# Kernel tuning notes

Hardware: AMD Instinct MI355X
Metric: run time of the kernel (lower is better)

Reference implementation:

```python
import jax, jax.numpy as jnp
import numpy as np

T, B, IN, H, OUT = 4096, 64, 4, 256, 2


def setup_inputs() -> dict:
    key = jax.random.key(0)
    ks = jax.random.split(key, 8)
    k = (1.0 / H) ** 0.5
    return {
        "input": jax.random.normal(ks[0], (T, B, IN), dtype=jnp.float32),
        "target": jax.random.normal(ks[1], (T, B, OUT), dtype=jnp.float32),
        "Wi": jax.random.uniform(ks[2], (H, IN), minval=-k, maxval=k, dtype=jnp.float32),
        "bi": jax.random.uniform(ks[3], (H,), minval=-k, maxval=k, dtype=jnp.float32),
        "Wh": jax.random.uniform(ks[4], (H, H), minval=-k, maxval=k, dtype=jnp.float32),
        "bh": jax.random.uniform(ks[5], (H,), minval=-k, maxval=k, dtype=jnp.float32),
        "Wf": jax.random.normal(ks[6], (OUT, H), dtype=jnp.float32) * (1.0 / H) ** 0.5,
        "bf": jnp.zeros((OUT,), dtype=jnp.float32),
    }


def reference(input, target, Wi, bi, Wh, bh, Wf, bf):
    # Precompute input projection for all timesteps: [T, B, H]
    xi = jnp.einsum("tbi,hi->tbh", input, Wi) + bi

    def step(h, xt):
        # h: [B, H]; xt: [B, H] (already projected input)
        h_new = jnp.tanh(xt + h @ Wh.T + bh)
        return h_new, h_new

    h0 = jnp.zeros((input.shape[1], Wh.shape[0]), dtype=input.dtype)
    _, hs = jax.lax.scan(step, h0, xi)  # hs: [T, B, H]

    # Output head: tanh(Linear(hidden)) -> [T, B, OUT]
    out = jnp.tanh(jnp.einsum("tbh,oh->tbo", hs, Wf) + bf)
    return out
```

## Files before the change

kernel.cpp:

```cpp
#include <hip/hip_runtime.h>

#define T_STEPS 4096
#define BATCH   64
#define INDIM   4
#define H       256
#define OUTD    2
#define CHUNK   32
#define SLOT_DW 36
#define ENT_DW  (4*SLOT_DW)
#define ENT_B   (4*ENT_DW)
#define RING_DW (CHUNK*ENT_DW)
#define WF_DW   (OUTD*(H/2))
#define XS_DW   (CHUNK*INDIM)

typedef __fp16 half2v __attribute__((ext_vector_type(2)));

__device__ __forceinline__ float fast_tanh(float x) {
    float ax = fabsf(x);
    float e  = __expf(-2.0f * ax);
    float r  = (1.0f - e) * __builtin_amdgcn_rcpf(1.0f + e);
    return copysignf(r, x);
}

template<int CTRL>
__device__ __forceinline__ float qadd(float a) {
    int s = __builtin_amdgcn_update_dpp(0, __builtin_bit_cast(int, a),
                                        CTRL, 0xf, 0xf, true);
    return a + __builtin_bit_cast(float, s);
}
#define QX1 0xB1
#define QX2 0x4E

__global__ __attribute__((amdgpu_waves_per_eu(1, 1))) __launch_bounds__(256)
void elman_kernel(const float* __restrict__ input,
                  const float* __restrict__ Wi,
                  const float* __restrict__ bi,
                  const float* __restrict__ Wh,
                  const float* __restrict__ bh,
                  const float* __restrict__ Wf,
                  const float* __restrict__ bf,
                  float* __restrict__ out)
{
    const int b  = blockIdx.x;
    const int t  = threadIdx.x;
    const int q  = t >> 2;
    const int ko = t & 3;
    const int k0 = ko * 64;

    __shared__ unsigned int lds[RING_DW + WF_DW + XS_DW];
    unsigned int* ring   = lds;
    unsigned int* wf_pk  = lds + RING_DW;
    float*        xstage = (float*)(lds + RING_DW + WF_DW);

    half2v w[4][32];
    #pragma unroll
    for (int r = 0; r < 4; ++r) {
        const float* p = Wh + (size_t)(4 * q + r) * H + k0;
        #pragma unroll
        for (int j = 0; j < 16; ++j) {
            float4 a = *(const float4*)(p + 4 * j);
            w[r][2 * j]     = __builtin_amdgcn_cvt_pkrtz(a.x, a.y);
            w[r][2 * j + 1] = __builtin_amdgcn_cvt_pkrtz(a.z, a.w);
        }
    }
    #pragma unroll
    for (int r = 0; r < 4; ++r)
        #pragma unroll
        for (int j = 0; j < 32; ++j) {
            float f = __builtin_bit_cast(float, w[r][j]);
            asm volatile("" : "+v"(f));
            w[r][j] = __builtin_bit_cast(half2v, f);
        }

    const float4 wim   = *(const float4*)(Wi + t * INDIM);
    const float  biasm = bi[t] + bh[t];
    const float  bf0   = bf[0], bf1 = bf[1];
    const int    boff  = (t >> 6) * (SLOT_DW * 4) + (t & 63) * 2;

    {
        const int o = t >> 7, e = t & 127;
        wf_pk[t] = __builtin_bit_cast(unsigned int,
            __builtin_amdgcn_cvt_pkrtz(Wf[o * H + 2 * e], Wf[o * H + 2 * e + 1]));
    }
    if (t < H / 2) ring[(CHUNK - 1) * ENT_DW + (t >> 5) * SLOT_DW + (t & 31)] = 0u;
    __syncthreads();

    const unsigned int rd_off = (unsigned int)(ko * SLOT_DW);

    for (int chunk = 0; chunk < T_STEPS / CHUNK; ++chunk) {
        if (t < CHUNK) {
            const int s = chunk * CHUNK + t;
            ((float4*)xstage)[t] = *(const float4*)(input + ((size_t)s * BATCH + b) * INDIM);
        }
        __syncthreads();

        #pragma unroll 1
        for (int i = 0; i < CHUNK; ++i) {
            const unsigned int* hb =
                ring + ((i + CHUNK - 1) & (CHUNK - 1)) * ENT_DW + rd_off;
            uint4 hv[8];
            #pragma unroll
            for (int j = 0; j < 8; ++j) hv[j] = *(const uint4*)(hb + 4 * j);
            const float4 xs = *((const float4*)xstage + i);

            float acc0 = 0.f, acc1 = 0.f, acc2 = 0.f, acc3 = 0.f;
            #pragma unroll
            for (int j = 0; j < 8; ++j) {
                half2v h0 = __builtin_bit_cast(half2v, hv[j].x);
                half2v h1 = __builtin_bit_cast(half2v, hv[j].y);
                half2v h2 = __builtin_bit_cast(half2v, hv[j].z);
                half2v h3 = __builtin_bit_cast(half2v, hv[j].w);
                acc0 = __builtin_amdgcn_fdot2(w[0][4 * j],     h0, acc0, false);
                acc1 = __builtin_amdgcn_fdot2(w[1][4 * j],     h0, acc1, false);
                acc2 = __builtin_amdgcn_fdot2(w[2][4 * j],     h0, acc2, false);
                acc3 = __builtin_amdgcn_fdot2(w[3][4 * j],     h0, acc3, false);
                acc0 = __builtin_amdgcn_fdot2(w[0][4 * j + 1], h1, acc0, false);
                acc1 = __builtin_amdgcn_fdot2(w[1][4 * j + 1], h1, acc1, false);
                acc2 = __builtin_amdgcn_fdot2(w[2][4 * j + 1], h1, acc2, false);
                acc3 = __builtin_amdgcn_fdot2(w[3][4 * j + 1], h1, acc3, false);
                acc0 = __builtin_amdgcn_fdot2(w[0][4 * j + 2], h2, acc0, false);
                acc1 = __builtin_amdgcn_fdot2(w[1][4 * j + 2], h2, acc1, false);
                acc2 = __builtin_amdgcn_fdot2(w[2][4 * j + 2], h2, acc2, false);
                acc3 = __builtin_amdgcn_fdot2(w[3][4 * j + 2], h2, acc3, false);
                acc0 = __builtin_amdgcn_fdot2(w[0][4 * j + 3], h3, acc0, false);
                acc1 = __builtin_amdgcn_fdot2(w[1][4 * j + 3], h3, acc1, false);
                acc2 = __builtin_amdgcn_fdot2(w[2][4 * j + 3], h3, acc2, false);
                acc3 = __builtin_amdgcn_fdot2(w[3][4 * j + 3], h3, acc3, false);
            }

            acc0 = qadd<QX1>(acc0);
            acc1 = qadd<QX1>(acc1);
            acc2 = qadd<QX1>(acc2);
            acc3 = qadd<QX1>(acc3);
            float A  = (ko & 1) ? acc1 : acc0;
            float Bv = (ko & 1) ? acc3 : acc2;
            A  = qadd<QX2>(A);
            Bv = qadd<QX2>(Bv);
            float accm = (ko & 2) ? Bv : A;

            float pre = accm + biasm +
                xs.x * wim.x + xs.y * wim.y + xs.z * wim.z + xs.w * wim.w;
            __fp16 h16 = (__fp16)fast_tanh(pre);
            *(__fp16*)((char*)ring + i * ENT_B + boff) = h16;

            __syncthreads();
        }

        {
            const int task = t >> 2;
            const int s    = task >> 1;
            const int o    = task & 1;
            const int sub  = t & 3;
            const unsigned int* hp = ring + s * ENT_DW + sub * SLOT_DW;
            const unsigned int* wp = wf_pk + o * (H / 2) + sub * 32;

            float acc = 0.f;
            #pragma unroll
            for (int j = 0; j < 8; ++j) {
                uint4 hq = *(const uint4*)(hp + 4 * j);
                uint4 wq = *(const uint4*)(wp + 4 * j);
                acc = __builtin_amdgcn_fdot2(__builtin_bit_cast(half2v, wq.x),
                                             __builtin_bit_cast(half2v, hq.x), acc, false);
                acc = __builtin_amdgcn_fdot2(__builtin_bit_cast(half2v, wq.y),
                                             __builtin_bit_cast(half2v, hq.y), acc, false);
                acc = __builtin_amdgcn_fdot2(__builtin_bit_cast(half2v, wq.z),
                                             __builtin_bit_cast(half2v, hq.z), acc, false);
                acc = __builtin_amdgcn_fdot2(__builtin_bit_cast(half2v, wq.w),
                                             __builtin_bit_cast(half2v, hq.w), acc, false);
            }
            acc = qadd<QX1>(acc);
            acc = qadd<QX2>(acc);

            if (sub == 0) {
                out[((size_t)(chunk * CHUNK + s) * BATCH + b) * OUTD + o] =
                    fast_tanh(acc + (o ? bf1 : bf0));
            }
            __syncthreads();
        }
    }
}

extern "C" void kernel_launch(void* const* d_in, const int* in_sizes, int n_in,
                              void* d_out, int out_size, void* d_ws, size_t ws_size,
                              hipStream_t stream) {
    const float* input = (const float*)d_in[0];
    const float* Wi = (const float*)d_in[2];
    const float* bi = (const float*)d_in[3];
    const float* bh = (const float*)d_in[5];
    const float* Wh = (const float*)d_in[4];
    const float* Wf = (const float*)d_in[6];
    const float* bf = (const float*)d_in[7];
    float* out = (float*)d_out;

    elman_kernel<<<dim3(BATCH), dim3(256), 0, stream>>>(
        input, Wi, bi, Wh, bh, Wf, bf, out);
}
```

Before: 1.821 ms.

## Split recurrent matvec across 8 lanes per 8-row group

Changes the thread-to-work mapping of the recurrent matvec. Each 8-lane group now owns 8 output rows and each lane covers a 32-element K slice, replacing the layout where each 4-lane group owned 4 rows over 64-element slices. The hidden-state ring uses 8 padded slices of 20 dwords, so each lane reads half as much from LDS per step. The cost is an extra DPP row-shift reduction stage and more selects. The Wf output head is adjusted to read the new slice layout.

```diff
diff --git a/kernel.cpp b/kernel.cpp
--- a/kernel.cpp
+++ b/kernel.cpp
@@ -6,14 +6,13 @@
 #define H       256
 #define OUTD    2
 #define CHUNK   32
-#define SLOT_DW 36
-#define ENT_DW  (4*SLOT_DW)
-#define ENT_B   (4*ENT_DW)
+#define SLICE_DW 20
+#define ENT_DW   168
 #define RING_DW (CHUNK*ENT_DW)
 #define WF_DW   (OUTD*(H/2))
 #define XS_DW   (CHUNK*INDIM)
 
-typedef __fp16 half2v __attribute__((ext_vector_type(2)));
+typedef _Float16 half2v __attribute__((ext_vector_type(2)));
 
 __device__ __forceinline__ float fast_tanh(float x) {
     float ax = fabsf(x);
@@ -28,8 +27,20 @@
                                         CTRL, 0xf, 0xf, true);
     return a + __builtin_bit_cast(float, s);
 }
-#define QX1 0xB1
-#define QX2 0x4E
+template<int CTRL>
+__device__ __forceinline__ float dppmov(float a) {
+    int s = __builtin_amdgcn_update_dpp(0, __builtin_bit_cast(int, a),
+                                        CTRL, 0xf, 0xf, true);
+    return __builtin_bit_cast(float, s);
+}
+#define QX1  0xB1
+#define QX2  0x4E
+#define RSHL4 0x104
+#define RSHR4 0x114
+
+__device__ __forceinline__ half2v pkh(float a, float b) {
+    return __builtin_bit_cast(half2v, __builtin_amdgcn_cvt_pkrtz(a, b));
+}
 
 __global__ __attribute__((amdgpu_waves_per_eu(1, 1))) __launch_bounds__(256)
 void elman_kernel(const float* __restrict__ input,
@@ -43,31 +54,31 @@
 {
     const int b  = blockIdx.x;
     const int t  = threadIdx.x;
-    const int q  = t >> 2;
-    const int ko = t & 3;
-    const int k0 = ko * 64;
+    const int Q  = t >> 3;
+    const int o  = t & 7;
+    const int k0 = o * 32;
 
     __shared__ unsigned int lds[RING_DW + WF_DW + XS_DW];
     unsigned int* ring   = lds;
     unsigned int* wf_pk  = lds + RING_DW;
     float*        xstage = (float*)(lds + RING_DW + WF_DW);
 
-    half2v w[4][32];
+    half2v w[8][16];
     #pragma unroll
-    for (int r = 0; r < 4; ++r) {
-        const float* p = Wh + (size_t)(4 * q + r) * H + k0;
+    for (int r = 0; r < 8; ++r) {
+        const float* p = Wh + (size_t)(8 * Q + r) * H + k0;
+        #pragma unroll
+        for (int m = 0; m < 8; ++m) {
+            float4 a = *(const float4*)(p + 4 * m);
+            w[r][2 * m]     = pkh(a.x, a.y);
+            w[r][2 * m + 1] = pkh(a.z, a.w);
+        }
+    }
+    #pragma unroll
+    for (int r = 0; r < 8; ++r)
         #pragma unroll
         for (int j = 0; j < 16; ++j) {
-            float4 a = *(const float4*)(p + 4 * j);
-            w[r][2 * j]     = __builtin_amdgcn_cvt_pkrtz(a.x, a.y);
-            w[r][2 * j + 1] = __builtin_amdgcn_cvt_pkrtz(a.z, a.w);
-        }
-    }
-    #pragma unroll
-    for (int r = 0; r < 4; ++r)
-        #pragma unroll
-        for (int j = 0; j < 32; ++j) {
-            float f = __builtin_bit_cast(float, w[r][j]);
+            int f = __builtin_bit_cast(int, w[r][j]);
             asm volatile("" : "+v"(f));
             w[r][j] = __builtin_bit_cast(half2v, f);
         }
@@ -75,17 +86,17 @@
     const float4 wim   = *(const float4*)(Wi + t * INDIM);
     const float  biasm = bi[t] + bh[t];
     const float  bf0   = bf[0], bf1 = bf[1];
-    const int    boff  = (t >> 6) * (SLOT_DW * 4) + (t & 63) * 2;
+    const int    boff  = (t >> 5) * (SLICE_DW * 4) + (t & 31) * 2;
 
     {
-        const int o = t >> 7, e = t & 127;
+        const int oc = t >> 7, e = t & 127;
         wf_pk[t] = __builtin_bit_cast(unsigned int,
-            __builtin_amdgcn_cvt_pkrtz(Wf[o * H + 2 * e], Wf[o * H + 2 * e + 1]));
+            __builtin_amdgcn_cvt_pkrtz(Wf[oc * H + 2 * e], Wf[oc * H + 2 * e + 1]));
     }
-    if (t < H / 2) ring[(CHUNK - 1) * ENT_DW + (t >> 5) * SLOT_DW + (t & 31)] = 0u;
+    if (t < ENT_DW) ring[(CHUNK - 1) * ENT_DW + t] = 0u;
     __syncthreads();
 
-    const unsigned int rd_off = (unsigned int)(ko * SLOT_DW);
+    const unsigned int rd_off = (unsigned int)(o * SLICE_DW);
 
     for (int chunk = 0; chunk < T_STEPS / CHUNK; ++chunk) {
         if (t < CHUNK) {
@@ -98,50 +109,58 @@
         for (int i = 0; i < CHUNK; ++i) {
             const unsigned int* hb =
                 ring + ((i + CHUNK - 1) & (CHUNK - 1)) * ENT_DW + rd_off;
-            uint4 hv[8];
-            #pragma unroll
-            for (int j = 0; j < 8; ++j) hv[j] = *(const uint4*)(hb + 4 * j);
+            uint4 hv[4];
+            #pragma unroll
+            for (int j = 0; j < 4; ++j) hv[j] = *(const uint4*)(hb + 4 * j);
             const float4 xs = *((const float4*)xstage + i);
 
-            float acc0 = 0.f, acc1 = 0.f, acc2 = 0.f, acc3 = 0.f;
-            #pragma unroll
-            for (int j = 0; j < 8; ++j) {
+            float accf[8];
+            #pragma unroll
+            for (int r = 0; r < 8; ++r) accf[r] = 0.f;
+            #pragma unroll
+            for (int j = 0; j < 4; ++j) {
                 half2v h0 = __builtin_bit_cast(half2v, hv[j].x);
                 half2v h1 = __builtin_bit_cast(half2v, hv[j].y);
                 half2v h2 = __builtin_bit_cast(half2v, hv[j].z);
                 half2v h3 = __builtin_bit_cast(half2v, hv[j].w);
-                acc0 = __builtin_amdgcn_fdot2(w[0][4 * j],     h0, acc0, false);
-                acc1 = __builtin_amdgcn_fdot2(w[1][4 * j],     h0, acc1, false);
-                acc2 = __builtin_amdgcn_fdot2(w[2][4 * j],     h0, acc2, false);
-                acc3 = __builtin_amdgcn_fdot2(w[3][4 * j],     h0, acc3, false);
-                acc0 = __builtin_amdgcn_fdot2(w[0][4 * j + 1], h1, acc0, false);
-                acc1 = __builtin_amdgcn_fdot2(w[1][4 * j + 1], h1, acc1, false);
-                acc2 = __builtin_amdgcn_fdot2(w[2][4 * j + 1], h1, acc2, false);
-                acc3 = __builtin_amdgcn_fdot2(w[3][4 * j + 1], h1, acc3, false);
-                acc0 = __builtin_amdgcn_fdot2(w[0][4 * j + 2], h2, acc0, false);
-                acc1 = __builtin_amdgcn_fdot2(w[1][4 * j + 2], h2, acc1, false);
-                acc2 = __builtin_amdgcn_fdot2(w[2][4 * j + 2], h2, acc2, false);
-                acc3 = __builtin_amdgcn_fdot2(w[3][4 * j + 2], h2, acc3, false);
-                acc0 = __builtin_amdgcn_fdot2(w[0][4 * j + 3], h3, acc0, false);
-                acc1 = __builtin_amdgcn_fdot2(w[1][4 * j + 3], h3, acc1, false);
-                acc2 = __builtin_amdgcn_fdot2(w[2][4 * j + 3], h3, acc2, false);
-                acc3 = __builtin_amdgcn_fdot2(w[3][4 * j + 3], h3, acc3, false);
-            }
-
-            acc0 = qadd<QX1>(acc0);
-            acc1 = qadd<QX1>(acc1);
-            acc2 = qadd<QX1>(acc2);
-            acc3 = qadd<QX1>(acc3);
-            float A  = (ko & 1) ? acc1 : acc0;
-            float Bv = (ko & 1) ? acc3 : acc2;
-            A  = qadd<QX2>(A);
-            Bv = qadd<QX2>(Bv);
-            float accm = (ko & 2) ? Bv : A;
+                #pragma unroll
+                for (int r = 0; r < 8; ++r)
+                    accf[r] = __builtin_amdgcn_fdot2(w[r][4 * j],     h0, accf[r], false);
+                #pragma unroll
+                for (int r = 0; r < 8; ++r)
+                    accf[r] = __builtin_amdgcn_fdot2(w[r][4 * j + 1], h1, accf[r], false);
+                #pragma unroll
+                for (int r = 0; r < 8; ++r)
+                    accf[r] = __builtin_amdgcn_fdot2(w[r][4 * j + 2], h2, accf[r], false);
+                #pragma unroll
+                for (int r = 0; r < 8; ++r)
+                    accf[r] = __builtin_amdgcn_fdot2(w[r][4 * j + 3], h3, accf[r], false);
+            }
+
+            #pragma unroll
+            for (int r = 0; r < 8; ++r) accf[r] = qadd<QX1>(accf[r]);
+            float s4_0 = (o & 1) ? accf[1] : accf[0];
+            float s4_1 = (o & 1) ? accf[3] : accf[2];
+            float s4_2 = (o & 1) ? accf[5] : accf[4];
+            float s4_3 = (o & 1) ? accf[7] : accf[6];
+            s4_0 = qadd<QX2>(s4_0);
+            s4_1 = qadd<QX2>(s4_1);
+            s4_2 = qadd<QX2>(s4_2);
+            s4_3 = qadd<QX2>(s4_3);
+            float s0 = (o & 2) ? s4_1 : s4_0;
+            float s1 = (o & 2) ? s4_3 : s4_2;
+            {
+                float u0 = dppmov<RSHL4>(s0), v0 = dppmov<RSHR4>(s0);
+                float u1 = dppmov<RSHL4>(s1), v1 = dppmov<RSHR4>(s1);
+                s0 += (o & 4) ? v0 : u0;
+                s1 += (o & 4) ? v1 : u1;
+            }
+            float accm = (o & 4) ? s1 : s0;
 
             float pre = accm + biasm +
                 xs.x * wim.x + xs.y * wim.y + xs.z * wim.z + xs.w * wim.w;
             __fp16 h16 = (__fp16)fast_tanh(pre);
-            *(__fp16*)((char*)ring + i * ENT_B + boff) = h16;
+            *(__fp16*)((char*)ring + i * (ENT_DW * 4) + boff) = h16;
 
             __syncthreads();
         }
@@ -149,15 +168,17 @@
         {
             const int task = t >> 2;
             const int s    = task >> 1;
-            const int o    = task & 1;
+            const int oc   = task & 1;
             const int sub  = t & 3;
-            const unsigned int* hp = ring + s * ENT_DW + sub * SLOT_DW;
-            const unsigned int* wp = wf_pk + o * (H / 2) + sub * 32;
+            const unsigned int* hp = ring + s * ENT_DW + sub * 2 * SLICE_DW;
+            const unsigned int* wp = wf_pk + oc * (H / 2) + sub * 32;
 
             float acc = 0.f;
             #pragma unroll
             for (int j = 0; j < 8; ++j) {
-                uint4 hq = *(const uint4*)(hp + 4 * j);
+                const unsigned int* hj = (j < 4) ? (hp + 4 * j)
+                                                 : (hp + SLICE_DW + 4 * (j - 4));
+                uint4 hq = *(const uint4*)(hj);
                 uint4 wq = *(const uint4*)(wp + 4 * j);
                 acc = __builtin_amdgcn_fdot2(__builtin_bit_cast(half2v, wq.x),
                                              __builtin_bit_cast(half2v, hq.x), acc, false);
@@ -172,8 +193,8 @@
             acc = qadd<QX2>(acc);
 
             if (sub == 0) {
-                out[((size_t)(chunk * CHUNK + s) * BATCH + b) * OUTD + o] =
-                    fast_tanh(acc + (o ? bf1 : bf0));
+                out[((size_t)(chunk * CHUNK + s) * BATCH + b) * OUTD + oc] =
+                    fast_tanh(acc + (oc ? bf1 : bf0));
             }
             __syncthreads();
         }
@@ -186,8 +207,8 @@
     const float* input = (const float*)d_in[0];
     const float* Wi = (const float*)d_in[2];
     const float* bi = (const float*)d_in[3];
+    const float* Wh = (const float*)d_in[4];
     const float* bh = (const float*)d_in[5];
-    const float* Wh = (const float*)d_in[4];
     const float* Wf = (const float*)d_in[6];
     const float* bf = (const float*)d_in[7];
     float* out = (float*)d_out;
```

Result: slower. 1.892 ms (+3.9%).
